# Kernel optimization log

Measured on AMD Instinct MI355X. Metric: run time of the kernel, lower is better.

Reference implementation:

```python
import jax, jax.numpy as jnp
import numpy as np

B, S, E, H = 2, 2048, 2048, 16
D = E // H

def setup_inputs() -> dict:
    key = jax.random.key(0)
    ks = jax.random.split(key, 9)
    sc = 1.0 / np.sqrt(E)
    return {
        "x":  jax.random.normal(ks[0], (B, S, E), jnp.float32),
        "Wq": jax.random.normal(ks[1], (E, E), jnp.float32) * sc,
        "bq": jax.random.normal(ks[2], (E,), jnp.float32) * 0.01,
        "Wk": jax.random.normal(ks[3], (E, E), jnp.float32) * sc,
        "bk": jax.random.normal(ks[4], (E,), jnp.float32) * 0.01,
        "Wv": jax.random.normal(ks[5], (E, E), jnp.float32) * sc,
        "bv": jax.random.normal(ks[6], (E,), jnp.float32) * 0.01,
        "Wo": jax.random.normal(ks[7], (E, E), jnp.float32) * sc,
        "bo": jax.random.normal(ks[8], (E,), jnp.float32) * 0.01,
    }

def _split_heads(t):
    # [B,S,E] -> [B,H,S,D]
    return t.reshape(B, S, H, D).transpose(0, 2, 1, 3)

def reference(x, Wq, bq, Wk, bk, Wv, bv, Wo, bo):
    # projections (nn.Linear: y = x @ W^T + b)
    q = _split_heads(x @ Wq.T + bq)
    k = _split_heads(x @ Wk.T + bk)
    v = _split_heads(x @ Wv.T + bv)

    # scaled causal attention; scale uses k.size(-1) == head_dim D
    scores = jnp.einsum("bhqd,bhkd->bhqk", q, k) / jnp.sqrt(jnp.asarray(D, q.dtype))
    causal = jnp.tril(jnp.ones((S, S), bool))  # [S,S]
    scores = jnp.where(causal[None, None, :, :], scores, -jnp.inf)
    # training path subtracts row max before softmax (no-op under stable softmax)
    scores = scores - jnp.max(scores, axis=-1, keepdims=True)
    attn = jax.nn.softmax(scores, axis=-1)
    # dropout_rate = 0.0 -> identity
    ctx = jnp.einsum("bhqk,bhkd->bhqd", attn, v)

    # merge heads [B,H,S,D] -> [B,S,E], final projection
    out = ctx.transpose(0, 2, 1, 3).reshape(B, S, E)
    return out @ Wo.T + bo
```

## Files before the change

### kernel.cpp

```cpp
#include <hip/hip_runtime.h>

typedef unsigned short u16;
typedef __attribute__((ext_vector_type(4))) float f32x4;
typedef __attribute__((ext_vector_type(8))) short s16x8;
typedef __attribute__((ext_vector_type(4))) unsigned short u16x4;

#define MFMA16(a, b, c) __builtin_amdgcn_mfma_f32_16x16x32_bf16((a), (b), (c), 0, 0, 0)

__device__ __forceinline__ u16 f2bf(float f) {
  union { float f; unsigned u; } v; v.f = f;
  unsigned u = v.u;
  u += 0x7fffu + ((u >> 16) & 1u);
  return (u16)(u >> 16);
}

__device__ __forceinline__ void gl_lds16(const void* g, void* l) {
  __builtin_amdgcn_global_load_lds(
      (const __attribute__((address_space(1))) void*)g,
      (__attribute__((address_space(3))) void*)l, 16, 0, 0);
}

__global__ void cast6(const float* __restrict__ x,
                      const float* __restrict__ w0, const float* __restrict__ w1,
                      const float* __restrict__ w2, const float* __restrict__ w3,
                      u16* __restrict__ ws) {
  const int y = blockIdx.y;
  const float* src;
  u16* dst;
  if (y < 2) { src = x + (size_t)y * 4194304; dst = ws + (size_t)y * 4194304; }
  else {
    src = (y == 2) ? w0 : (y == 3) ? w1 : (y == 4) ? w2 : w3;
    dst = ws + 8388608 + (size_t)(y - 2) * 4194304;
  }
  const int i = blockIdx.x * 256 + threadIdx.x;
  f32x4 v = ((const f32x4*)src)[i];
  u16x4 o;
#pragma unroll
  for (int e = 0; e < 4; ++e) o[e] = f2bf(v[e]);
  ((u16x4*)dst)[i] = o;
}

template <int SWAP>
__device__ __forceinline__ void gemm_core(const u16* __restrict__ A,
                                          const u16* __restrict__ Bw,
                                          u16* sA, u16* sB,
                                          f32x4 (&acc)[4][4],
                                          int m0, int n0, int tid) {
  const int lane = tid & 63, w = tid >> 6;
  const int ln = lane & 15, quad = lane >> 4, ln7 = ln & 7;
  const int wm = (w >> 1) * 64, wn = (w & 1) * 64;
  const int srow = lane >> 3;
  const int scol = (((lane & 7) ^ srow)) * 8;

  for (int k0 = 0; k0 < 2048; k0 += 64) {
#pragma unroll
    for (int c = 0; c < 4; ++c) {
      const int chunk = c * 4 + w;
      const int row = chunk * 8 + srow;
      gl_lds16(A + (size_t)(m0 + row) * 2048 + k0 + scol, (char*)sA + chunk * 1024);
      gl_lds16(Bw + (size_t)(n0 + row) * 2048 + k0 + scol, (char*)sB + chunk * 1024);
    }
    __syncthreads();
#pragma unroll
    for (int kk = 0; kk < 64; kk += 32) {
      s16x8 af[4], bf[4];
      const int g = (kk >> 3) + quad;
#pragma unroll
      for (int t = 0; t < 4; ++t) {
        af[t] = *(const s16x8*)&sA[(wm + t * 16 + ln) * 64 + ((g ^ ln7) << 3)];
        bf[t] = *(const s16x8*)&sB[(wn + t * 16 + ln) * 64 + ((g ^ ln7) << 3)];
      }
#pragma unroll
      for (int tm = 0; tm < 4; ++tm)
#pragma unroll
        for (int tn = 0; tn < 4; ++tn)
          acc[tm][tn] = SWAP ? MFMA16(bf[tn], af[tm], acc[tm][tn])
                             : MFMA16(af[tm], bf[tn], acc[tm][tn]);
    }
    __syncthreads();
  }
}

__global__ __launch_bounds__(256, 2) void gemm_qkv(
    const u16* __restrict__ A,
    const u16* __restrict__ W0, const u16* __restrict__ W1, const u16* __restrict__ W2,
    const float* __restrict__ b0, const float* __restrict__ b1, const float* __restrict__ b2,
    u16* __restrict__ Qo, u16* __restrict__ Ko, u16* __restrict__ Vo) {
  __shared__ __align__(16) u16 smem[16384];
  u16* sA = smem;
  u16* sB = smem + 8192;
  const int z = blockIdx.z;
  const u16* Bw = (z == 0) ? W0 : (z == 1) ? W1 : W2;
  const float* bias = (z == 0) ? b0 : (z == 1) ? b1 : b2;

  const int tid = threadIdx.x;
  const int lane = tid & 63, w = tid >> 6;
  const int ln = lane & 15, quad = lane >> 4;
  const int m0 = blockIdx.y * 128, n0 = blockIdx.x * 128;
  const int wm = (w >> 1) * 64, wn = (w & 1) * 64;

  f32x4 acc[4][4] = {};
  if (z < 2) {
    gemm_core<1>(A, Bw, sA, sB, acc, m0, n0, tid);
    u16* out = (z == 0) ? Qo : Ko;
    const float scale = (z == 0) ? 0.08838834764831845f : 1.0f;
#pragma unroll
    for (int tn = 0; tn < 4; ++tn) {
      const int n_base = n0 + wn + tn * 16 + quad * 4;
      const f32x4 bv = *(const f32x4*)&bias[n_base];
      const int h = n_base >> 7, dl = n_base & 127;
#pragma unroll
      for (int tm = 0; tm < 4; ++tm) {
        const int m = m0 + wm + tm * 16 + ln;
        const int b = m >> 11, s = m & 2047;
        u16x4 ov;
#pragma unroll
        for (int r = 0; r < 4; ++r) ov[r] = f2bf((acc[tm][tn][r] + bv[r]) * scale);
        *(u16x4*)&out[(((size_t)(b * 16 + h)) << 18) + ((size_t)s << 7) + dl] = ov;
      }
    }
  } else {
    gemm_core<0>(A, Bw, sA, sB, acc, m0, n0, tid);
    const int b = m0 >> 11;
#pragma unroll
    for (int tn = 0; tn < 4; ++tn) {
      const int n = n0 + wn + tn * 16 + ln;
      const float bv = bias[n];
      const int h = n >> 7, dl = n & 127;
#pragma unroll
      for (int tm = 0; tm < 4; ++tm) {
        const int s_base = (m0 & 2047) + wm + tm * 16 + quad * 4;
        u16x4 ov;
#pragma unroll
        for (int r = 0; r < 4; ++r) ov[r] = f2bf(acc[tm][tn][r] + bv);
        *(u16x4*)&Vo[(((size_t)((b * 16 + h) * 128 + dl)) << 11) + s_base] = ov;
      }
    }
  }
}

__global__ __launch_bounds__(256, 2) void gemm_out(const u16* __restrict__ A,
                                                   const u16* __restrict__ Bw,
                                                   const float* __restrict__ bias,
                                                   float* __restrict__ out) {
  __shared__ __align__(16) u16 smem[16384];
  u16* sA = smem;
  u16* sB = smem + 8192;
  const int tid = threadIdx.x;
  const int lane = tid & 63, w = tid >> 6;
  const int ln = lane & 15, quad = lane >> 4;
  const int m0 = blockIdx.y * 128, n0 = blockIdx.x * 128;
  const int wm = (w >> 1) * 64, wn = (w & 1) * 64;

  f32x4 acc[4][4] = {};
  gemm_core<1>(A, Bw, sA, sB, acc, m0, n0, tid);
#pragma unroll
  for (int tn = 0; tn < 4; ++tn) {
    const int n_base = n0 + wn + tn * 16 + quad * 4;
    const f32x4 bv = *(const f32x4*)&bias[n_base];
#pragma unroll
    for (int tm = 0; tm < 4; ++tm) {
      const int m = m0 + wm + tm * 16 + ln;
      f32x4 ov;
#pragma unroll
      for (int r = 0; r < 4; ++r) ov[r] = acc[tm][tn][r] + bv[r];
      *(f32x4*)&out[(size_t)m * 2048 + n_base] = ov;
    }
  }
}

__global__ __launch_bounds__(256, 2) void attn_kernel(const u16* __restrict__ Q,
                                                      const u16* __restrict__ Kp,
                                                      const u16* __restrict__ Vt,
                                                      u16* __restrict__ ctx) {
  __shared__ __align__(16) u16 smem[24576];
  u16* sP = smem;
  u16* sK = smem + 8192;
  u16* sV = smem + 16384;

  const int flat = blockIdx.x + (blockIdx.y << 4);
  const int bh = flat >> 4;
  const int i = (flat < 256) ? (15 - (flat & 15)) : (flat & 15);
  const size_t base = (size_t)bh << 18;

  const int tid = threadIdx.x, lane = tid & 63, w = tid >> 6;
  const int ln = lane & 15, quad = lane >> 4, ln7 = lane & 7;

#pragma unroll
  for (int c = 0; c < 8; ++c) {
    const int chunk0 = (c * 4 + w) * 64;
    const int chunk = chunk0 + lane;
    const int row = chunk >> 4, cc = chunk & 15;
    gl_lds16(Q + base + (size_t)((i * 128 + row) * 128 + ((cc ^ (row & 15)) << 3)),
             (char*)sK + chunk0 * 16);
  }
  __syncthreads();
  s16x8 qf[2][4];
#pragma unroll
  for (int qt = 0; qt < 2; ++qt)
#pragma unroll
    for (int kc = 0; kc < 4; ++kc)
      qf[qt][kc] =
          *(const s16x8*)&sK[(w * 32 + qt * 16 + ln) * 128 + (((kc * 4 + quad) ^ ln) << 3)];
  __syncthreads();

  auto stageK = [&](int j) {
#pragma unroll
    for (int c = 0; c < 4; ++c) {
      const int chunk0 = (c * 4 + w) * 64;
      const int chunk = chunk0 + lane;
      const int row = chunk >> 4, cc = chunk & 15;
      gl_lds16(Kp + base + (size_t)((j * 64 + row) * 128 + ((cc ^ (row & 15)) << 3)),
               (char*)sK + chunk0 * 16);
    }
  };
  auto stageV = [&](int j) {
#pragma unroll
    for (int c = 0; c < 4; ++c) {
      const int chunk0 = (c * 4 + w) * 64;
      const int chunk = chunk0 + lane;
      const int row = chunk >> 3, cc = chunk & 7;
      gl_lds16(Vt + base + (size_t)(row * 2048 + j * 64 + ((cc ^ (row & 7)) << 3)),
               (char*)sV + chunk0 * 16);
    }
  };

  stageK(0);
  stageV(0);
  __syncthreads();

  f32x4 o_acc[8][2] = {};
  float lsum[2] = {0.f, 0.f};
  const int jmax = 2 * i + 1;
  const int qg = i * 128 + w * 32 + ln;

  for (int j = 0; j <= jmax; ++j) {
    f32x4 sacc[4][2] = {};
#pragma unroll
    for (int kc = 0; kc < 4; ++kc) {
      s16x8 kf[4];
#pragma unroll
      for (int kt = 0; kt < 4; ++kt)
        kf[kt] = *(const s16x8*)&sK[(kt * 16 + ln) * 128 + (((kc * 4 + quad) ^ ln) << 3)];
#pragma unroll
      for (int kt = 0; kt < 4; ++kt)
#pragma unroll
        for (int qt = 0; qt < 2; ++qt)
          sacc[kt][qt] = MFMA16(kf[kt], qf[qt][kc], sacc[kt][qt]);
    }

    const bool diag = (j >= 2 * i);
#pragma unroll
    for (int kt = 0; kt < 4; ++kt)
#pragma unroll
      for (int qt = 0; qt < 2; ++qt) {
        u16x4 pk;
#pragma unroll
        for (int r = 0; r < 4; ++r) {
          const int kg = j * 64 + kt * 16 + quad * 4 + r;
          float pv = __expf(sacc[kt][qt][r]);
          if (diag && kg > qg + qt * 16) pv = 0.f;
          lsum[qt] += pv;
          pk[r] = f2bf(pv);
        }
        const int qrow = w * 32 + qt * 16 + ln;
        const int c = kt * 4 + quad;
        *(u16x4*)&sP[qrow * 64 + ((c ^ (qrow & 14)) << 2)] = pk;
      }
    __syncthreads();
    if (j < jmax) stageK(j + 1);

#pragma unroll
    for (int kc = 0; kc < 2; ++kc) {
      s16x8 vf[8], pf[2];
#pragma unroll
      for (int qt = 0; qt < 2; ++qt) {
        const int qrow = w * 32 + qt * 16 + ln;
        const int c0 = kc * 8 + quad * 2;
        pf[qt] = *(const s16x8*)&sP[qrow * 64 + ((c0 ^ (qrow & 14)) << 2)];
      }
#pragma unroll
      for (int dt = 0; dt < 8; ++dt)
        vf[dt] = *(const s16x8*)&sV[(dt * 16 + ln) * 64 + (((kc * 4 + quad) ^ ln7) << 3)];
#pragma unroll
      for (int dt = 0; dt < 8; ++dt)
#pragma unroll
        for (int qt = 0; qt < 2; ++qt)
          o_acc[dt][qt] = MFMA16(vf[dt], pf[qt], o_acc[dt][qt]);
    }
    __syncthreads();
    if (j < jmax) stageV(j + 1);
  }

  const int b = bh >> 4, h = bh & 15;
  float rinv[2];
#pragma unroll
  for (int qt = 0; qt < 2; ++qt) {
    float s = lsum[qt];
    s += __shfl_xor(s, 16);
    s += __shfl_xor(s, 32);
    rinv[qt] = __builtin_amdgcn_rcpf(s);
  }
#pragma unroll
  for (int dt = 0; dt < 8; ++dt)
#pragma unroll
    for (int qt = 0; qt < 2; ++qt) {
      const int sg = i * 128 + w * 32 + qt * 16 + ln;
      const int d0 = h * 128 + dt * 16 + quad * 4;
      u16x4 ov;
#pragma unroll
      for (int r = 0; r < 4; ++r) ov[r] = f2bf(o_acc[dt][qt][r] * rinv[qt]);
      *(u16x4*)&ctx[((size_t)b << 22) + (size_t)sg * 2048 + d0] = ov;
    }
}

extern "C" void kernel_launch(void* const* d_in, const int* in_sizes, int n_in,
                              void* d_out, int out_size, void* d_ws, size_t ws_size,
                              hipStream_t stream) {
  const float* x = (const float*)d_in[0];
  const float* Wq = (const float*)d_in[1];
  const float* bq = (const float*)d_in[2];
  const float* Wk = (const float*)d_in[3];
  const float* bk = (const float*)d_in[4];
  const float* Wv = (const float*)d_in[5];
  const float* bv = (const float*)d_in[6];
  const float* Wo = (const float*)d_in[7];
  const float* bo = (const float*)d_in[8];

  u16* ws = (u16*)d_ws;
  u16* xb = ws;
  u16* Wqb = xb + 8388608;
  u16* Wkb = Wqb + 4194304;
  u16* Wvb = Wkb + 4194304;
  u16* Wob = Wvb + 4194304;
  u16* Qb = Wob + 4194304;
  u16* Kb = Qb + 8388608;
  u16* Vtb = Kb + 8388608;
  u16* ctxb = Vtb + 8388608;

  cast6<<<dim3(4096, 6), 256, 0, stream>>>(x, Wq, Wk, Wv, Wo, ws);

  gemm_qkv<<<dim3(16, 32, 3), 256, 0, stream>>>(xb, Wqb, Wkb, Wvb, bq, bk, bv, Qb, Kb, Vtb);

  attn_kernel<<<dim3(16, 32), 256, 0, stream>>>(Qb, Kb, Vtb, ctxb);

  gemm_out<<<dim3(16, 32), 256, 0, stream>>>(ctxb, Wob, bo, (float*)d_out);
}
```

Before: 363.5 us.

## Use 256x256 tiles with a 4-stage async LDS pipeline for QKV GEMM

Replaces the 128x128 QKV projection GEMM with a 256x256 tile per 512-thread block. The new core streams K in 32-wide slices through a 4-deep ring of LDS buffers filled by direct global-to-LDS loads, using explicit waitcnt and barriers, and raises wave priority around the MFMA bursts. The larger tiles raise arithmetic intensity and the pipelining hides load latency. In exchange it uses 128 KB of LDS per block and more accumulator registers, and the grid shrinks to 384 blocks, which limits occupancy and may leave the CUs unevenly loaded.

```diff
diff --git a/kernel.cpp b/kernel.cpp
--- a/kernel.cpp
+++ b/kernel.cpp
@@ -81,14 +81,92 @@
   }
 }
 
-__global__ __launch_bounds__(256, 2) void gemm_qkv(
+template <int SWAP>
+__device__ __forceinline__ void gemm_core256(const u16* __restrict__ A,
+                                             const u16* __restrict__ Bw,
+                                             u16* smem,
+                                             f32x4 (&acc)[8][4],
+                                             int m0, int n0, int tid) {
+  const int lane = tid & 63, w = tid >> 6;
+  const int ln = lane & 15, quad = lane >> 4;
+  const int wm = (w >> 2) << 7;
+  const int wn = (w & 3) << 6;
+  const int sr = tid >> 2;
+  const int ssw = (((tid & 3) ^ ((sr >> 1) & 3)) << 3);
+  const int swq = ((quad ^ ((ln >> 1) & 3)) << 3);
+  const int wofs = w << 9;
+
+  const u16* Asrc = A + (size_t)(m0 + sr) * 2048 + ssw;
+  const u16* Bsrc = Bw + (size_t)(n0 + sr) * 2048 + ssw;
+
+  auto STAGE = [&](int t) {
+    u16* sl = smem + ((t & 3) << 14);
+    const int k0 = t << 5;
+    gl_lds16(Asrc + k0,                sl + wofs);
+    gl_lds16(Asrc + k0 + 128 * 2048,   sl + 4096 + wofs);
+    gl_lds16(Bsrc + k0,                sl + 8192 + wofs);
+    gl_lds16(Bsrc + k0 + 128 * 2048,   sl + 12288 + wofs);
+  };
+
+  auto COMPUTE = [&](int t) {
+    const u16* sl = smem + ((t & 3) << 14);
+    s16x8 af[8], bf[4];
+#pragma unroll
+    for (int j = 0; j < 4; ++j)
+      bf[j] = *(const s16x8*)&sl[8192 + (wn + j * 16 + ln) * 32 + swq];
+#pragma unroll
+    for (int tt = 0; tt < 8; ++tt)
+      af[tt] = *(const s16x8*)&sl[(wm + tt * 16 + ln) * 32 + swq];
+    __builtin_amdgcn_s_setprio(1);
+#pragma unroll
+    for (int tt = 0; tt < 8; ++tt)
+#pragma unroll
+      for (int j = 0; j < 4; ++j)
+        acc[tt][j] = SWAP ? MFMA16(bf[j], af[tt], acc[tt][j])
+                          : MFMA16(af[tt], bf[j], acc[tt][j]);
+    __builtin_amdgcn_s_setprio(0);
+  };
+
+  STAGE(0); STAGE(1); STAGE(2);
+
+#define STEP(T)                                                       \
+  asm volatile("s_waitcnt vmcnt(8) lgkmcnt(0)" ::: "memory");         \
+  __builtin_amdgcn_s_barrier();                                       \
+  asm volatile("" ::: "memory");                                      \
+  STAGE((T) + 3);                                                     \
+  COMPUTE(T);
+
+  int t = 0;
+#pragma unroll 1
+  for (int tb = 0; tb < 15; ++tb, t += 4) {
+    STEP(t + 0)
+    STEP(t + 1)
+    STEP(t + 2)
+    STEP(t + 3)
+  }
+  STEP(60)
+#undef STEP
+
+  asm volatile("s_waitcnt vmcnt(8) lgkmcnt(0)" ::: "memory");
+  __builtin_amdgcn_s_barrier();
+  asm volatile("" ::: "memory");
+  COMPUTE(61);
+  asm volatile("s_waitcnt vmcnt(4) lgkmcnt(0)" ::: "memory");
+  __builtin_amdgcn_s_barrier();
+  asm volatile("" ::: "memory");
+  COMPUTE(62);
+  asm volatile("s_waitcnt vmcnt(0) lgkmcnt(0)" ::: "memory");
+  __builtin_amdgcn_s_barrier();
+  asm volatile("" ::: "memory");
+  COMPUTE(63);
+}
+
+__global__ __launch_bounds__(512, 2) void gemm_qkv256(
     const u16* __restrict__ A,
     const u16* __restrict__ W0, const u16* __restrict__ W1, const u16* __restrict__ W2,
     const float* __restrict__ b0, const float* __restrict__ b1, const float* __restrict__ b2,
     u16* __restrict__ Qo, u16* __restrict__ Ko, u16* __restrict__ Vo) {
-  __shared__ __align__(16) u16 smem[16384];
-  u16* sA = smem;
-  u16* sB = smem + 8192;
+  __shared__ __align__(16) u16 smem[65536];
   const int z = blockIdx.z;
   const u16* Bw = (z == 0) ? W0 : (z == 1) ? W1 : W2;
   const float* bias = (z == 0) ? b0 : (z == 1) ? b1 : b2;
@@ -96,12 +174,12 @@
   const int tid = threadIdx.x;
   const int lane = tid & 63, w = tid >> 6;
   const int ln = lane & 15, quad = lane >> 4;
-  const int m0 = blockIdx.y * 128, n0 = blockIdx.x * 128;
-  const int wm = (w >> 1) * 64, wn = (w & 1) * 64;
-
-  f32x4 acc[4][4] = {};
+  const int m0 = blockIdx.y * 256, n0 = blockIdx.x * 256;
+  const int wm = (w >> 2) << 7, wn = (w & 3) << 6;
+
+  f32x4 acc[8][4] = {};
   if (z < 2) {
-    gemm_core<1>(A, Bw, sA, sB, acc, m0, n0, tid);
+    gemm_core256<1>(A, Bw, smem, acc, m0, n0, tid);
     u16* out = (z == 0) ? Qo : Ko;
     const float scale = (z == 0) ? 0.08838834764831845f : 1.0f;
 #pragma unroll
@@ -110,7 +188,7 @@
       const f32x4 bv = *(const f32x4*)&bias[n_base];
       const int h = n_base >> 7, dl = n_base & 127;
 #pragma unroll
-      for (int tm = 0; tm < 4; ++tm) {
+      for (int tm = 0; tm < 8; ++tm) {
         const int m = m0 + wm + tm * 16 + ln;
         const int b = m >> 11, s = m & 2047;
         u16x4 ov;
@@ -120,7 +198,7 @@
       }
     }
   } else {
-    gemm_core<0>(A, Bw, sA, sB, acc, m0, n0, tid);
+    gemm_core256<0>(A, Bw, smem, acc, m0, n0, tid);
     const int b = m0 >> 11;
 #pragma unroll
     for (int tn = 0; tn < 4; ++tn) {
@@ -128,7 +206,7 @@
       const float bv = bias[n];
       const int h = n >> 7, dl = n & 127;
 #pragma unroll
-      for (int tm = 0; tm < 4; ++tm) {
+      for (int tm = 0; tm < 8; ++tm) {
         const int s_base = (m0 & 2047) + wm + tm * 16 + quad * 4;
         u16x4 ov;
 #pragma unroll
@@ -340,7 +418,7 @@
 
   cast6<<<dim3(4096, 6), 256, 0, stream>>>(x, Wq, Wk, Wv, Wo, ws);
 
-  gemm_qkv<<<dim3(16, 32, 3), 256, 0, stream>>>(xb, Wqb, Wkb, Wvb, bq, bk, bv, Qb, Kb, Vtb);
+  gemm_qkv256<<<dim3(8, 16, 3), 512, 0, stream>>>(xb, Wqb, Wkb, Wvb, bq, bk, bv, Qb, Kb, Vtb);
 
   attn_kernel<<<dim3(16, 32), 256, 0, stream>>>(Qb, Kb, Vtb, ctxb);
 
```

Measured after the change: 370.2 us. Within noise of the previous version (+1.8%).

## Replace QKV projection GEMM with 8-wave double-buffered pipelined kernel

Applied to the files above, without the earlier changes.

The fused QKV projection now uses a new 512-thread kernel that computes a 256x128 output tile per block, up from 128x128. Global-to-LDS loads of the next K-slices go into a second LDS buffer while MFMAs run on the current one. Explicit barriers, waitcnt and s_setprio split the work into quarter-tile phases so loads and matrix math overlap and waves take turns issuing. The cost is 96KB of LDS per block and half as many blocks, which lowers occupancy and relies on hand-placed vmcnt counts being correct.

```diff
diff --git a/kernel.cpp b/kernel.cpp
--- a/kernel.cpp
+++ b/kernel.cpp
@@ -81,14 +81,111 @@
   }
 }
 
-__global__ __launch_bounds__(256, 2) void gemm_qkv(
+template <int SWAP>
+__device__ __forceinline__ void gemm8p(const u16* __restrict__ A,
+                                       const u16* __restrict__ Bw,
+                                       u16* smem, f32x4 (&acc)[4][4],
+                                       int m0, int n0, int tid) {
+  const int lane = tid & 63, w = tid >> 6;
+  const int ln = lane & 15, quad = lane >> 4, ln7 = lane & 7;
+  const int sw0 = (quad ^ ln7) << 3, sw1 = ((4 + quad) ^ ln7) << 3;
+  const int srow = (w << 3) + (lane >> 3);
+  const int scc = ((lane & 7) ^ (lane >> 3)) << 3;
+  const u16* aRd = smem + (w >> 2) * 8192 + ((w >> 1) & 1) * 4096;
+  const u16* bRd = smem + 16384 + (w & 1) * 4096;
+  u16* dstW = smem + (w << 9);
+
+  s16x8 af[4][2], bf[4][2];
+
+  auto STG = [&](const u16* mat, int grow, int t, int dstu) {
+    const u16* s0 = mat + (size_t)(grow + srow) * 2048 + ((t & 31) << 6) + scc;
+    gl_lds16(s0, dstW + dstu);
+    gl_lds16(s0 + 64 * 2048, dstW + dstu + 4096);
+  };
+  auto RDA = [&](int bo, int tm0) {
+#pragma unroll
+    for (int u = 0; u < 2; ++u) {
+      const int tt = tm0 + u;
+      af[tt][0] = *(const s16x8*)&aRd[bo + (tt * 16 + ln) * 64 + sw0];
+      af[tt][1] = *(const s16x8*)&aRd[bo + (tt * 16 + ln) * 64 + sw1];
+    }
+  };
+  auto RDB = [&](int bo, int tn0) {
+#pragma unroll
+    for (int u = 0; u < 2; ++u) {
+      const int tt = tn0 + u;
+      bf[tt][0] = *(const s16x8*)&bRd[bo + (tt * 16 + ln) * 64 + sw0];
+      bf[tt][1] = *(const s16x8*)&bRd[bo + (tt * 16 + ln) * 64 + sw1];
+    }
+  };
+  auto QM = [&](int tm0, int tn0) {
+#pragma unroll
+    for (int tm = tm0; tm < tm0 + 2; ++tm)
+#pragma unroll
+      for (int tn = tn0; tn < tn0 + 2; ++tn)
+#pragma unroll
+        for (int ks = 0; ks < 2; ++ks)
+          acc[tm][tn] = SWAP ? MFMA16(bf[tn][ks], af[tm][ks], acc[tm][tn])
+                             : MFMA16(af[tm][ks], bf[tn][ks], acc[tm][tn]);
+  };
+
+#define PH_MID()                                             \
+  __builtin_amdgcn_s_barrier();                              \
+  asm volatile("s_waitcnt lgkmcnt(0)" ::: "memory");         \
+  __builtin_amdgcn_sched_barrier(0);                         \
+  __builtin_amdgcn_s_setprio(1)
+#define PH_END()                                             \
+  __builtin_amdgcn_s_setprio(0);                             \
+  __builtin_amdgcn_s_barrier()
+#define PH_ENDV()                                            \
+  __builtin_amdgcn_s_setprio(0);                             \
+  asm volatile("s_waitcnt vmcnt(4)" ::: "memory");           \
+  __builtin_amdgcn_s_barrier()
+
+  STG(A, m0, 0, 0);
+  STG(A, m0 + 128, 0, 8192);
+  STG(Bw, n0, 0, 16384);
+  STG(A, m0, 1, 24576);
+  STG(A, m0 + 128, 1, 24576 + 8192);
+  asm volatile("s_waitcnt vmcnt(4)" ::: "memory");
+  __builtin_amdgcn_s_barrier();
+
+#pragma unroll 1
+  for (int j = 0; j < 16; ++j) {
+    const int te = 2 * j + 2, to = 2 * j + 3;
+    RDA(0, 0); RDB(0, 0);
+    STG(Bw, n0, 2 * j + 1, 24576 + 16384);
+    PH_MID(); QM(0, 0); PH_END();
+    RDA(0, 2);
+    PH_MID(); QM(2, 0); PH_END();
+    RDB(0, 2);
+    STG(A, m0, te, 0);
+    PH_MID(); QM(2, 2); PH_END();
+    STG(A, m0 + 128, te, 8192);
+    PH_MID(); QM(0, 2); PH_ENDV();
+    RDA(24576, 0); RDB(24576, 0);
+    STG(Bw, n0, te, 16384);
+    PH_MID(); QM(0, 0); PH_END();
+    RDA(24576, 2);
+    PH_MID(); QM(2, 0); PH_END();
+    RDB(24576, 2);
+    STG(A, m0, to, 24576);
+    PH_MID(); QM(2, 2); PH_END();
+    STG(A, m0 + 128, to, 24576 + 8192);
+    PH_MID(); QM(0, 2); PH_ENDV();
+  }
+  asm volatile("s_waitcnt vmcnt(0)" ::: "memory");
+#undef PH_MID
+#undef PH_END
+#undef PH_ENDV
+}
+
+__global__ __launch_bounds__(512, 2) void gemm_qkv8(
     const u16* __restrict__ A,
     const u16* __restrict__ W0, const u16* __restrict__ W1, const u16* __restrict__ W2,
     const float* __restrict__ b0, const float* __restrict__ b1, const float* __restrict__ b2,
     u16* __restrict__ Qo, u16* __restrict__ Ko, u16* __restrict__ Vo) {
-  __shared__ __align__(16) u16 smem[16384];
-  u16* sA = smem;
-  u16* sB = smem + 8192;
+  __shared__ __align__(16) u16 smem[49152];
   const int z = blockIdx.z;
   const u16* Bw = (z == 0) ? W0 : (z == 1) ? W1 : W2;
   const float* bias = (z == 0) ? b0 : (z == 1) ? b1 : b2;
@@ -96,12 +193,12 @@
   const int tid = threadIdx.x;
   const int lane = tid & 63, w = tid >> 6;
   const int ln = lane & 15, quad = lane >> 4;
-  const int m0 = blockIdx.y * 128, n0 = blockIdx.x * 128;
+  const int m0 = blockIdx.y * 256, n0 = blockIdx.x * 128;
   const int wm = (w >> 1) * 64, wn = (w & 1) * 64;
 
   f32x4 acc[4][4] = {};
   if (z < 2) {
-    gemm_core<1>(A, Bw, sA, sB, acc, m0, n0, tid);
+    gemm8p<1>(A, Bw, smem, acc, m0, n0, tid);
     u16* out = (z == 0) ? Qo : Ko;
     const float scale = (z == 0) ? 0.08838834764831845f : 1.0f;
 #pragma unroll
@@ -120,7 +217,7 @@
       }
     }
   } else {
-    gemm_core<0>(A, Bw, sA, sB, acc, m0, n0, tid);
+    gemm8p<0>(A, Bw, smem, acc, m0, n0, tid);
     const int b = m0 >> 11;
 #pragma unroll
     for (int tn = 0; tn < 4; ++tn) {
@@ -340,7 +437,7 @@
 
   cast6<<<dim3(4096, 6), 256, 0, stream>>>(x, Wq, Wk, Wv, Wo, ws);
 
-  gemm_qkv<<<dim3(16, 32, 3), 256, 0, stream>>>(xb, Wqb, Wkb, Wvb, bq, bk, bv, Qb, Kb, Vtb);
+  gemm_qkv8<<<dim3(16, 16, 3), 512, 0, stream>>>(xb, Wqb, Wkb, Wvb, bq, bk, bv, Qb, Kb, Vtb);
 
   attn_kernel<<<dim3(16, 32), 256, 0, stream>>>(Qb, Kb, Vtb, ctxb);
 
```

Measured after the change: 360.4 us. Within noise of the previous version (-0.8%).

## Add 256x256 ping-pong pipelined GEMM for Q/K projections, split V GEMM

Applied to the files above, without the earlier changes.

Replaces the fused QKV projection kernel with a dedicated 256x256-tile, 512-thread GEMM for Q and K. It double-buffers global-to-LDS loads and interleaves MFMA phases with s_setprio and barriers to overlap loads with compute. The V projection moves to a separate launch that keeps the old 128x128 core because it writes a transposed layout. The larger tile cuts global traffic per FLOP, at the cost of 128 KB of LDS per block, an extra kernel launch, and lower occupancy.

```diff
diff --git a/kernel.cpp b/kernel.cpp
--- a/kernel.cpp
+++ b/kernel.cpp
@@ -81,18 +81,150 @@
   }
 }
 
-__global__ __launch_bounds__(256, 2) void gemm_qkv(
+__global__ __launch_bounds__(512, 2) void gemm_qk256(
     const u16* __restrict__ A,
-    const u16* __restrict__ W0, const u16* __restrict__ W1, const u16* __restrict__ W2,
-    const float* __restrict__ b0, const float* __restrict__ b1, const float* __restrict__ b2,
-    u16* __restrict__ Qo, u16* __restrict__ Ko, u16* __restrict__ Vo) {
+    const u16* __restrict__ W0, const u16* __restrict__ W1,
+    const float* __restrict__ b0, const float* __restrict__ b1,
+    u16* __restrict__ Qo, u16* __restrict__ Ko) {
+  __shared__ __align__(16) u16 smem[65536];
+  const int z = blockIdx.z;
+  const u16* Bw = z ? W1 : W0;
+  const float* bias = z ? b1 : b0;
+  u16* out = z ? Ko : Qo;
+  const float scale = z ? 1.0f : 0.08838834764831845f;
+
+  const int tid = threadIdx.x;
+  const int lane = tid & 63, w = tid >> 6;
+  const int ln = lane & 15, quad = lane >> 4, ln7 = lane & 7;
+  const int m0 = blockIdx.y * 256, n0 = blockIdx.x * 256;
+  const int wm = (w >> 2) << 7, wn = (w & 3) << 6;
+
+  const int ci0 = tid, ci1 = 512 + tid;
+  const int r0 = ci0 >> 3, c0k = ((ci0 & 7) ^ (r0 & 7)) << 3;
+  const int r1 = ci1 >> 3, c1k = ((ci1 & 7) ^ (r1 & 7)) << 3;
+  const int abase = (w >> 2) << 13;
+  const int bbase = 16384 + (((w >> 1) & 1) << 13) + ((w & 1) << 12);
+  const int sw0 = (quad ^ ln7) << 3, sw1 = ((4 + quad) ^ ln7) << 3;
+
+  f32x4 acc[8][4] = {};
+  s16x8 af[8][2], bf[4][2];
+
+  auto STGA = [&](int t) {
+    u16* dst = smem + ((t & 1) << 15);
+    const int kc = (t & 31) << 6;
+    const u16* s0 = A + (size_t)(m0 + r0) * 2048 + kc + c0k;
+    const u16* s1 = A + (size_t)(m0 + r1) * 2048 + kc + c1k;
+    gl_lds16(s0, dst + ci0 * 8);
+    gl_lds16(s1, dst + ci1 * 8);
+    gl_lds16(s0 + (size_t)128 * 2048, dst + 8192 + ci0 * 8);
+    gl_lds16(s1 + (size_t)128 * 2048, dst + 8192 + ci1 * 8);
+  };
+  auto STGB = [&](int t) {
+    u16* dst = smem + ((t & 1) << 15) + 16384;
+    const int kc = (t & 31) << 6;
+    const u16* s0 = Bw + (size_t)(n0 + r0) * 2048 + kc + c0k;
+    const u16* s1 = Bw + (size_t)(n0 + r1) * 2048 + kc + c1k;
+    gl_lds16(s0, dst + ci0 * 8);
+    gl_lds16(s1, dst + ci1 * 8);
+    gl_lds16(s0 + (size_t)128 * 2048, dst + 8192 + ci0 * 8);
+    gl_lds16(s1 + (size_t)128 * 2048, dst + 8192 + ci1 * 8);
+  };
+  auto RDA = [&](int buf, int tm0) {
+    const u16* p = smem + (buf << 15) + abase;
+#pragma unroll
+    for (int u = 0; u < 4; ++u) {
+      const int tt = tm0 + u;
+      af[tt][0] = *(const s16x8*)&p[(tt * 16 + ln) * 64 + sw0];
+      af[tt][1] = *(const s16x8*)&p[(tt * 16 + ln) * 64 + sw1];
+    }
+  };
+  auto RDB = [&](int buf, int tn0) {
+    const u16* p = smem + (buf << 15) + bbase;
+#pragma unroll
+    for (int u = 0; u < 2; ++u) {
+      const int tt = tn0 + u;
+      bf[tt][0] = *(const s16x8*)&p[(tt * 16 + ln) * 64 + sw0];
+      bf[tt][1] = *(const s16x8*)&p[(tt * 16 + ln) * 64 + sw1];
+    }
+  };
+  auto QM = [&](int tm0, int tn0) {
+#pragma unroll
+    for (int tm = tm0; tm < tm0 + 4; ++tm)
+#pragma unroll
+      for (int tn = tn0; tn < tn0 + 2; ++tn)
+#pragma unroll
+        for (int ks = 0; ks < 2; ++ks)
+          acc[tm][tn] = MFMA16(bf[tn][ks], af[tm][ks], acc[tm][tn]);
+  };
+
+#define PH_MID()                                             \
+  __builtin_amdgcn_s_barrier();                              \
+  asm volatile("s_waitcnt lgkmcnt(0)" ::: "memory");         \
+  __builtin_amdgcn_sched_barrier(0);                         \
+  __builtin_amdgcn_s_setprio(1)
+#define PH_END()                                             \
+  __builtin_amdgcn_s_setprio(0);                             \
+  __builtin_amdgcn_s_barrier()
+#define PH_ENDV()                                            \
+  __builtin_amdgcn_s_setprio(0);                             \
+  asm volatile("s_waitcnt vmcnt(4)" ::: "memory");           \
+  __builtin_amdgcn_s_barrier()
+
+  STGA(0); STGB(0); STGA(1);
+  asm volatile("s_waitcnt vmcnt(4)" ::: "memory");
+  __builtin_amdgcn_s_barrier();
+
+#pragma unroll 1
+  for (int j = 0; j < 16; ++j) {
+    const int t = 2 * j;
+    RDA(0, 0); RDB(0, 0);
+    STGB(t + 1);
+    PH_MID(); QM(0, 0); PH_END();
+    RDA(0, 4);
+    PH_MID(); QM(4, 0); PH_END();
+    RDB(0, 2);
+    PH_MID(); QM(4, 2); PH_END();
+    STGA(t + 2);
+    PH_MID(); QM(0, 2); PH_ENDV();
+    RDA(1, 0); RDB(1, 0);
+    STGB(t + 2);
+    PH_MID(); QM(0, 0); PH_END();
+    RDA(1, 4);
+    PH_MID(); QM(4, 0); PH_END();
+    RDB(1, 2);
+    PH_MID(); QM(4, 2); PH_END();
+    STGA(t + 3);
+    PH_MID(); QM(0, 2); PH_ENDV();
+  }
+  asm volatile("s_waitcnt vmcnt(0)" ::: "memory");
+#undef PH_MID
+#undef PH_END
+#undef PH_ENDV
+
+#pragma unroll
+  for (int tn = 0; tn < 4; ++tn) {
+    const int n_base = n0 + wn + tn * 16 + quad * 4;
+    const f32x4 bv = *(const f32x4*)&bias[n_base];
+    const int h = n_base >> 7, dl = n_base & 127;
+#pragma unroll
+    for (int tm = 0; tm < 8; ++tm) {
+      const int m = m0 + wm + tm * 16 + ln;
+      const int b = m >> 11, s = m & 2047;
+      u16x4 ov;
+#pragma unroll
+      for (int r = 0; r < 4; ++r) ov[r] = f2bf((acc[tm][tn][r] + bv[r]) * scale);
+      *(u16x4*)&out[(((size_t)(b * 16 + h)) << 18) + ((size_t)s << 7) + dl] = ov;
+    }
+  }
+}
+
+__global__ __launch_bounds__(256, 2) void gemm_v(const u16* __restrict__ A,
+                                                 const u16* __restrict__ Bw,
+                                                 const float* __restrict__ bias,
+                                                 u16* __restrict__ Vo) {
   __shared__ __align__(16) u16 smem[16384];
   u16* sA = smem;
   u16* sB = smem + 8192;
-  const int z = blockIdx.z;
-  const u16* Bw = (z == 0) ? W0 : (z == 1) ? W1 : W2;
-  const float* bias = (z == 0) ? b0 : (z == 1) ? b1 : b2;
-
   const int tid = threadIdx.x;
   const int lane = tid & 63, w = tid >> 6;
   const int ln = lane & 15, quad = lane >> 4;
@@ -100,41 +232,20 @@
   const int wm = (w >> 1) * 64, wn = (w & 1) * 64;
 
   f32x4 acc[4][4] = {};
-  if (z < 2) {
-    gemm_core<1>(A, Bw, sA, sB, acc, m0, n0, tid);
-    u16* out = (z == 0) ? Qo : Ko;
-    const float scale = (z == 0) ? 0.08838834764831845f : 1.0f;
-#pragma unroll
-    for (int tn = 0; tn < 4; ++tn) {
-      const int n_base = n0 + wn + tn * 16 + quad * 4;
-      const f32x4 bv = *(const f32x4*)&bias[n_base];
-      const int h = n_base >> 7, dl = n_base & 127;
-#pragma unroll
-      for (int tm = 0; tm < 4; ++tm) {
-        const int m = m0 + wm + tm * 16 + ln;
-        const int b = m >> 11, s = m & 2047;
-        u16x4 ov;
-#pragma unroll
-        for (int r = 0; r < 4; ++r) ov[r] = f2bf((acc[tm][tn][r] + bv[r]) * scale);
-        *(u16x4*)&out[(((size_t)(b * 16 + h)) << 18) + ((size_t)s << 7) + dl] = ov;
-      }
-    }
-  } else {
-    gemm_core<0>(A, Bw, sA, sB, acc, m0, n0, tid);
-    const int b = m0 >> 11;
-#pragma unroll
-    for (int tn = 0; tn < 4; ++tn) {
-      const int n = n0 + wn + tn * 16 + ln;
-      const float bv = bias[n];
-      const int h = n >> 7, dl = n & 127;
-#pragma unroll
-      for (int tm = 0; tm < 4; ++tm) {
-        const int s_base = (m0 & 2047) + wm + tm * 16 + quad * 4;
-        u16x4 ov;
-#pragma unroll
-        for (int r = 0; r < 4; ++r) ov[r] = f2bf(acc[tm][tn][r] + bv);
-        *(u16x4*)&Vo[(((size_t)((b * 16 + h) * 128 + dl)) << 11) + s_base] = ov;
-      }
+  gemm_core<0>(A, Bw, sA, sB, acc, m0, n0, tid);
+  const int b = m0 >> 11;
+#pragma unroll
+  for (int tn = 0; tn < 4; ++tn) {
+    const int n = n0 + wn + tn * 16 + ln;
+    const float bv = bias[n];
+    const int h = n >> 7, dl = n & 127;
+#pragma unroll
+    for (int tm = 0; tm < 4; ++tm) {
+      const int s_base = (m0 & 2047) + wm + tm * 16 + quad * 4;
+      u16x4 ov;
+#pragma unroll
+      for (int r = 0; r < 4; ++r) ov[r] = f2bf(acc[tm][tn][r] + bv);
+      *(u16x4*)&Vo[(((size_t)((b * 16 + h) * 128 + dl)) << 11) + s_base] = ov;
     }
   }
 }
@@ -340,7 +451,8 @@
 
   cast6<<<dim3(4096, 6), 256, 0, stream>>>(x, Wq, Wk, Wv, Wo, ws);
 
-  gemm_qkv<<<dim3(16, 32, 3), 256, 0, stream>>>(xb, Wqb, Wkb, Wvb, bq, bk, bv, Qb, Kb, Vtb);
+  gemm_qk256<<<dim3(8, 16, 2), 512, 0, stream>>>(xb, Wqb, Wkb, bq, bk, Qb, Kb);
+  gemm_v<<<dim3(16, 32), 256, 0, stream>>>(xb, Wvb, bv, Vtb);
 
   attn_kernel<<<dim3(16, 32), 256, 0, stream>>>(Qb, Kb, Vtb, ctxb);
 
```

Result: no change. 359.5 us (-1.1%).
